# Optimization experiments

Measured on AMD Instinct MI355X. Metric: run time of the kernel, lower is better.

The kernel has to match this reference:

```python
import jax, jax.numpy as jnp
import numpy as np
from jax import lax

B, CIN, LIN = 65536, 1, 274
D, S, H, NL = 16, 18, 4, 4
DH = D // H  # 4
HID = 64
EPS = 1e-5

def layer_norm(x, g, b):
    m = jnp.mean(x, axis=-1, keepdims=True)
    v = jnp.mean(jnp.square(x - m), axis=-1, keepdims=True)
    return (x - m) * lax.rsqrt(v + EPS) * g + b

def setup_inputs() -> dict:
    key = jax.random.key(0)
    ks = jax.random.split(key, 16)
    n = lambda k, shp, s=0.05: jax.random.normal(k, shp, dtype=jnp.float32) * s
    return {
        "x": jax.random.normal(ks[0], (B, CIN, LIN), dtype=jnp.float32),
        "patch_w": n(ks[1], (D, CIN, 16), 0.2),   # Conv1d weight (O,I,K)
        "patch_b": jnp.zeros((D,), jnp.float32),
        "pos_embed": n(ks[2], (1, S, D), 0.02),
        "ln1_g": jnp.ones((NL, D), jnp.float32),
        "ln1_b": jnp.zeros((NL, D), jnp.float32),
        "qkv_w": n(ks[3], (NL, 3 * D, D), 0.2),    # in_proj_weight per layer
        "qkv_b": jnp.zeros((NL, 3 * D), jnp.float32),
        "out_w": n(ks[4], (NL, D, D), 0.2),
        "out_b": jnp.zeros((NL, D), jnp.float32),
        "ln2_g": jnp.ones((NL, D), jnp.float32),
        "ln2_b": jnp.zeros((NL, D), jnp.float32),
        "mlp_w1": n(ks[5], (NL, HID, D), 0.2),
        "mlp_b1": jnp.zeros((NL, HID), jnp.float32),
        "mlp_w2": n(ks[6], (NL, D, HID), 0.2),
        "mlp_b2": jnp.zeros((NL, D), jnp.float32),
        "lnf_g": jnp.ones((D,), jnp.float32),
        "lnf_b": jnp.zeros((D,), jnp.float32),
        "dec_w": n(ks[7], (D, CIN, 16), 0.2),      # ConvTranspose1d weight (I,O,K)
        "dec_b": jnp.zeros((CIN,), jnp.float32),
    }

def reference(x, patch_w, patch_b, pos_embed, ln1_g, ln1_b, qkv_w, qkv_b,
              out_w, out_b, ln2_g, ln2_b, mlp_w1, mlp_b1, mlp_w2, mlp_b2,
              lnf_g, lnf_b, dec_w, dec_b):
    dn = ('NCH', 'OIH', 'NCH')
    # patchify: (B,1,274) -> (B,16,18) -> (B,18,16)
    h = lax.conv_general_dilated(x, patch_w, (16,), [(7, 7)], dimension_numbers=dn)
    h = h + patch_b[None, :, None]
    h = jnp.transpose(h, (0, 2, 1)) + pos_embed
    scale = 1.0 / np.sqrt(DH)
    for i in range(NL):
        xn = layer_norm(h, ln1_g[i], ln1_b[i])
        qkv = xn @ qkv_w[i].T + qkv_b[i]                      # (B,S,3D)
        q, k, v = jnp.split(qkv, 3, axis=-1)
        q = q.reshape(B, S, H, DH)
        k = k.reshape(B, S, H, DH)
        v = v.reshape(B, S, H, DH)
        att = jnp.einsum('bqhd,bkhd->bhqk', q, k) * scale
        att = jax.nn.softmax(att, axis=-1)
        o = jnp.einsum('bhqk,bkhd->bqhd', att, v).reshape(B, S, D)
        h = h + (o @ out_w[i].T + out_b[i])
        xn2 = layer_norm(h, ln2_g[i], ln2_b[i])
        m = jax.nn.gelu(xn2 @ mlp_w1[i].T + mlp_b1[i], approximate=False)
        h = h + (m @ mlp_w2[i].T + mlp_b2[i])
    h = layer_norm(h, lnf_g, lnf_b)
    z = jnp.transpose(h, (0, 2, 1))                            # (B,16,18)
    # ConvTranspose1d(k=16, s=16, p=7): lhs_dilation=16, pad=k-1-p=8, flipped kernel
    w_t = jnp.transpose(jnp.flip(dec_w, axis=-1), (1, 0, 2))   # (O=1, I=16, 16)
    out = lax.conv_general_dilated(z, w_t, (1,), [(8, 8)], lhs_dilation=(16,),
                                   dimension_numbers=dn)
    out = out + dec_b[None, :, None]                            # (B,1,274)
    return out, z
```

## Files before the change

kernel.cpp:

```cpp
#include <hip/hip_runtime.h>
#include <math.h>
#include <stdint.h>

#define NB      65536
#define LIN     274
#define SEQ     18
#define DM      16
#define NH      4
#define HID     64
#define NLAYER  4
#define EPSF    1e-5f

#define EPB      8
#define NTHREADS 192
#define BUF_DW   3488
#define VOFF_DW  1152
#define VSTR     292
#define SMEM_DW  (2 * BUF_DW)

#define QS 0.72134752044448170f

typedef _Float16 h2    __attribute__((ext_vector_type(2)));
typedef _Float16 f16x4 __attribute__((ext_vector_type(4)));
typedef _Float16 f16x8 __attribute__((ext_vector_type(8)));
typedef float    f32x4 __attribute__((ext_vector_type(4)));
typedef __fp16   hf2_raw __attribute__((ext_vector_type(2)));

#if __has_builtin(__builtin_amdgcn_fdot2)
__device__ __forceinline__ float fdot2(h2 a, h2 b, float c) { return __builtin_amdgcn_fdot2(a, b, c, false); }
#else
__device__ __forceinline__ float fdot2(h2 a, h2 b, float c) { return c + (float)a[0] * (float)b[0] + (float)a[1] * (float)b[1]; }
#endif
#if __has_builtin(__builtin_amdgcn_cvt_pkrtz)
__device__ __forceinline__ h2 pkrtz(float a, float b) {
    hf2_raw r = __builtin_amdgcn_cvt_pkrtz(a, b);
    return __builtin_bit_cast(h2, r);
}
#else
__device__ __forceinline__ h2 pkrtz(float a, float b) { h2 r; r[0] = (_Float16)a; r[1] = (_Float16)b; return r; }
#endif

#if __has_builtin(__builtin_amdgcn_mfma_f32_16x16x16f16)
__device__ __forceinline__ f32x4 MFMA16(f16x4 a, f16x4 b, f32x4 c) {
    return __builtin_amdgcn_mfma_f32_16x16x16f16(a, b, c, 0, 0, 0);
}
#elif __has_builtin(__builtin_amdgcn_mfma_f32_16x16x16_f16)
__device__ __forceinline__ f32x4 MFMA16(f16x4 a, f16x4 b, f32x4 c) {
    return __builtin_amdgcn_mfma_f32_16x16x16_f16(a, b, c, 0, 0, 0);
}
#else
__device__ __forceinline__ f32x4 MFMA16(f16x4 a, f16x4 b, f32x4 c) {
    f32x4 d;
    asm volatile("v_mfma_f32_16x16x16_f16 %0, %1, %2, %3"
                 : "=v"(d) : "v"(a), "v"(b), "v"(c));
    return d;
}
#endif

__device__ __forceinline__ float fast_rcp(float x)  { return __builtin_amdgcn_rcpf(x); }
__device__ __forceinline__ float fast_rsq(float x)  { return __builtin_amdgcn_rsqf(x); }
__device__ __forceinline__ float fast_exp2(float x) { return __builtin_amdgcn_exp2f(x); }

__device__ __forceinline__ float bfly16_32(float x) {
#if __has_builtin(__builtin_amdgcn_permlane16_swap) && __has_builtin(__builtin_amdgcn_permlane32_swap)
    unsigned u = __builtin_bit_cast(unsigned, x);
    auto p16 = __builtin_amdgcn_permlane16_swap(u, u, false, false);
    float s = __builtin_bit_cast(float, (unsigned)p16[0]) + __builtin_bit_cast(float, (unsigned)p16[1]);
    unsigned v = __builtin_bit_cast(unsigned, s);
    auto p32 = __builtin_amdgcn_permlane32_swap(v, v, false, false);
    return __builtin_bit_cast(float, (unsigned)p32[0]) + __builtin_bit_cast(float, (unsigned)p32[1]);
#else
    x += __shfl_xor(x, 16);
    x += __shfl_xor(x, 32);
    return x;
#endif
}

__device__ __forceinline__ float gelu_tanh(float t) {
    const float A2 = 0.79788456080286536f * 2.88539008177792681f;
    const float B2 = 0.03567740814183430f * 2.88539008177792681f;
    float u  = t * fmaf(t * t, B2, A2);
    float e  = fast_exp2(u);
    float r  = fast_rcp(e + 1.0f);
    return fmaf(-t, r, t);
}

__device__ __forceinline__ f16x4 pk4(float a, float b, float c, float d) {
    h2 lo = pkrtz(a, b), hi = pkrtz(c, d);
    f16x4 r; r[0] = lo[0]; r[1] = lo[1]; r[2] = hi[0]; r[3] = hi[1];
    return r;
}
__device__ __forceinline__ f32x4 ld4(const float* p) {
    float4 t = *(const float4*)p;
    f32x4 r; r[0] = t.x; r[1] = t.y; r[2] = t.z; r[3] = t.w;
    return r;
}
__device__ __forceinline__ h2 h2at(f16x8 v, int i) {
    h2 r; r[0] = v[2 * i]; r[1] = v[2 * i + 1]; return r;
}

#define WS_H2_COUNT 6400
#define WS_BIAS_FLOATS (NLAYER * 112)
#define WS_TOTAL_BYTES (WS_H2_COUNT * 4 + WS_BIAS_FLOATS * 4)
#define PREP_ITEMS (WS_H2_COUNT + WS_BIAS_FLOATS)

__global__ __launch_bounds__(512) void prep_weights(
    const float* __restrict__ patch_w, const float* __restrict__ dec_w,
    const float* __restrict__ qkv_w, const float* __restrict__ out_w,
    const float* __restrict__ mlp_w1, const float* __restrict__ mlp_w2,
    const float* __restrict__ ln1_g, const float* __restrict__ ln1_b,
    const float* __restrict__ ln2_g, const float* __restrict__ ln2_b,
    const float* __restrict__ qkv_b, const float* __restrict__ mlp_b1,
    h2* __restrict__ ws)
{
    int i = blockIdx.x * 512 + threadIdx.x;
    if (i >= PREP_ITEMS) return;
    if (i < WS_H2_COUNT) {
        int tile = i >> 7;
        int lane = (i >> 1) & 63;
        int p    = i & 1;
        int row  = lane & 15;
        int kb   = (lane >> 4) * 4 + 2 * p;
        float a, b;
        if (tile == 0)      { a = patch_w[row * 16 + kb];  b = patch_w[row * 16 + kb + 1]; }
        else if (tile == 1) { a = dec_w[kb * 16 + row];    b = dec_w[(kb + 1) * 16 + row]; }
        else {
            int t2 = tile - 2, li = t2 / 12, j = t2 % 12;
            const float* s;
            float g0 = 1.0f, g1v = 1.0f;
            if (j < 3) {
                s = qkv_w + li * 768 + (j * 16 + row) * 16 + kb;
                g0 = ln1_g[li * 16 + kb]; g1v = ln1_g[li * 16 + kb + 1];
                if (j == 0) { g0 *= QS; g1v *= QS; }
            } else if (j == 3) {
                s = out_w + li * 256 + row * 16 + kb;
            } else if (j < 8) {
                s = mlp_w1 + li * 1024 + ((j - 4) * 16 + row) * 16 + kb;
                g0 = ln2_g[li * 16 + kb]; g1v = ln2_g[li * 16 + kb + 1];
            } else {
                s = mlp_w2 + li * 1024 + row * 64 + (j - 8) * 16 + kb;
            }
            a = s[0] * g0; b = s[1] * g1v;
        }
        ws[i] = pkrtz(a, b);
    } else {
        int t = i - WS_H2_COUNT;
        int li = t / 112, r = t % 112;
        float* wbf = (float*)(ws + WS_H2_COUNT);
        float bv;
        if (r < 48) {
            const float* Wr = qkv_w + li * 768 + r * 16;
            const float* lb = ln1_b + li * 16;
            bv = qkv_b[li * 48 + r];
            for (int d = 0; d < 16; ++d) bv = fmaf(Wr[d], lb[d], bv);
            if (r < 16) bv *= QS;
        } else {
            int j = r - 48;
            const float* Wr = mlp_w1 + li * 1024 + j * 16;
            const float* lb = ln2_b + li * 16;
            bv = mlp_b1[li * 64 + j];
            for (int d = 0; d < 16; ++d) bv = fmaf(Wr[d], lb[d], bv);
        }
        wbf[li * 112 + r] = bv;
    }
}

__global__ __launch_bounds__(NTHREADS) void ae_fwd(
    const float* __restrict__ x,
    const float* __restrict__ patch_b, const float* __restrict__ pos_embed,
    const h2*    __restrict__ wp, const float* __restrict__ wb,
    const float* __restrict__ out_b, const float* __restrict__ mlp_b2,
    const float* __restrict__ lnf_g, const float* __restrict__ lnf_b,
    const float* __restrict__ dec_b,
    float* __restrict__ out_y, float* __restrict__ out_z)
{
    __shared__ float smem[SMEM_DW];
    const int tid  = threadIdx.x;
    const int lane = tid & 63;
    const int wv   = tid >> 6;
    const int col  = lane & 15;
    const int g16  = lane >> 4;
    const int fb   = g16 * 4;

    {
        const float4* xg = (const float4*)(x + (long long)blockIdx.x * (EPB * LIN));
        float4* xs = (float4*)(smem + BUF_DW);
        for (int i = tid; i < (EPB * LIN) / 4; i += NTHREADS) xs[i] = xg[i];
    }
    __syncthreads();

    int elemL[3], sIdx[3];
    #pragma unroll
    for (int t = 0; t < 3; ++t) {
        int T = wv * 48 + t * 16 + col;
        int e = (T * 57) >> 10;
        elemL[t] = e;
        sIdx[t]  = T - 18 * e;
    }

    const f16x4* wfrag = (const f16x4*)wp;
    const f16x4 wpatch = wfrag[lane];
    const f16x4 wdec   = wfrag[64 + lane];

    float hacc[3][4];
    {
        const float4 pb = *(const float4*)(patch_b + fb);
        const float* xst = smem + BUF_DW;
        #pragma unroll
        for (int t = 0; t < 3; ++t) {
            float xv[4];
            #pragma unroll
            for (int r = 0; r < 4; ++r) {
                int loc = sIdx[t] * 16 - 7 + fb + r;
                xv[r] = (loc >= 0 && loc < LIN) ? xst[elemL[t] * LIN + loc] : 0.0f;
            }
            f16x4 xb = pk4(xv[0], xv[1], xv[2], xv[3]);
            const float4 pe = *(const float4*)(pos_embed + sIdx[t] * DM + fb);
            f32x4 c; c[0] = pb.x + pe.x; c[1] = pb.y + pe.y; c[2] = pb.z + pe.z; c[3] = pb.w + pe.w;
            c = MFMA16(wpatch, xb, c);
            #pragma unroll
            for (int r = 0; r < 4; ++r) hacc[t][r] = c[r];
        }
    }

    #pragma unroll 1
    for (int li = 0; li < NLAYER; ++li) {
        const int bufO = (li & 1) ? BUF_DW : 0;
        const f16x4* wl = wfrag + (2 + li * 12) * 64 + lane;
        const float* wbL = wb + li * 112;
        const f32x4 bq = ld4(wbL + fb);
        const f32x4 bk = ld4(wbL + 16 + fb);
        const f32x4 bvx = ld4(wbL + 32 + fb);
        f32x4 b1r[4];
        #pragma unroll
        for (int c = 0; c < 4; ++c) b1r[c] = ld4(wbL + 48 + c * 16 + fb);
        const float4 ob4 = *(const float4*)(out_b + li * DM + fb);
        const f32x4 b2r = ld4(mlp_b2 + li * DM + fb);

        h2 qp[3][2]; f16x4 kpk[3]; f32x4 vreg[3];
        #pragma unroll
        for (int t = 0; t < 3; ++t) {
            float a0 = hacc[t][0], a1 = hacc[t][1], a2 = hacc[t][2], a3 = hacc[t][3];
            float sm = bfly16_32(a0 + a1 + a2 + a3);
            float qq = bfly16_32(fmaf(a0, a0, fmaf(a1, a1, fmaf(a2, a2, a3 * a3))));
            float mean = sm * (1.0f / 16.0f);
            float var  = fmaxf(fmaf(mean, -mean, qq * (1.0f / 16.0f)), 0.0f);
            float inv  = fast_rsq(var + EPSF);
            float mi   = mean * inv;
            f16x4 xb = pk4(fmaf(a0, inv, -mi), fmaf(a1, inv, -mi),
                           fmaf(a2, inv, -mi), fmaf(a3, inv, -mi));
            f32x4 aq = MFMA16(wl[0],   xb, bq);
            f32x4 ak = MFMA16(wl[64],  xb, bk);
            f32x4 av = MFMA16(wl[128], xb, bvx);
            qp[t][0] = pkrtz(aq[0], aq[1]);
            qp[t][1] = pkrtz(aq[2], aq[3]);
            kpk[t] = pk4(ak[0], ak[1], ak[2], ak[3]);
            vreg[t] = av;
        }
        #pragma unroll
        for (int t = 0; t < 3; ++t) {
            ((f16x4*)(smem + bufO))[(elemL[t] * 4 + g16) * 18 + sIdx[t]] = kpk[t];
            float4 vv; vv.x = vreg[t][0]; vv.y = vreg[t][1]; vv.z = vreg[t][2]; vv.w = vreg[t][3];
            *(float4*)(smem + bufO + VOFF_DW + elemL[t] * VSTR + sIdx[t] * 16 + g16 * 4) = vv;
        }
        __syncthreads();

        #pragma unroll
        for (int t = 0; t < 3; ++t) {
            const int e = elemL[t];
            const f16x4* Kb = (const f16x4*)(smem + bufO) + (e * 4 + g16) * 18;
            float sc[SEQ]; float ssum = 0.0f;
            #pragma unroll
            for (int jp = 0; jp < 9; ++jp) {
                f16x8 k2 = *(const f16x8*)(Kb + 2 * jp);
                float s0 = fdot2(qp[t][1], h2at(k2, 1), fdot2(qp[t][0], h2at(k2, 0), 0.0f));
                float s1 = fdot2(qp[t][1], h2at(k2, 3), fdot2(qp[t][0], h2at(k2, 2), 0.0f));
                float w0 = fast_exp2(s0), w1 = fast_exp2(s1);
                sc[2 * jp] = w0; sc[2 * jp + 1] = w1;
                ssum += w0 + w1;
            }
            float inv = fast_rcp(ssum);
            const float* vb = smem + bufO + VOFF_DW + e * VSTR + g16 * 4;
            float o0 = 0.f, o1 = 0.f, o2 = 0.f, o3 = 0.f;
            #pragma unroll
            for (int j = 0; j < SEQ; ++j) {
                float4 vj = *(const float4*)(vb + j * 16);
                float w = sc[j];
                o0 = fmaf(w, vj.x, o0); o1 = fmaf(w, vj.y, o1);
                o2 = fmaf(w, vj.z, o2); o3 = fmaf(w, vj.w, o3);
            }
            f16x4 obf = pk4(o0 * inv, o1 * inv, o2 * inv, o3 * inv);
            f32x4 oa; oa[0] = ob4.x; oa[1] = ob4.y; oa[2] = ob4.z; oa[3] = ob4.w;
            oa = MFMA16(wl[192], obf, oa);
            #pragma unroll
            for (int r = 0; r < 4; ++r) hacc[t][r] += oa[r];
        }

        #pragma unroll
        for (int t = 0; t < 3; ++t) {
            float a0 = hacc[t][0], a1 = hacc[t][1], a2 = hacc[t][2], a3 = hacc[t][3];
            float sm = bfly16_32(a0 + a1 + a2 + a3);
            float qq = bfly16_32(fmaf(a0, a0, fmaf(a1, a1, fmaf(a2, a2, a3 * a3))));
            float mean = sm * (1.0f / 16.0f);
            float var  = fmaxf(fmaf(mean, -mean, qq * (1.0f / 16.0f)), 0.0f);
            float inv  = fast_rsq(var + EPSF);
            float mi   = mean * inv;
            f16x4 xb2 = pk4(fmaf(a0, inv, -mi), fmaf(a1, inv, -mi),
                            fmaf(a2, inv, -mi), fmaf(a3, inv, -mi));
            f32x4 acc2 = b2r;
            #pragma unroll
            for (int c = 0; c < 4; ++c) {
                f32x4 m1 = MFMA16(wl[(4 + c) * 64], xb2, b1r[c]);
                f16x4 gb = pk4(gelu_tanh(m1[0]), gelu_tanh(m1[1]),
                               gelu_tanh(m1[2]), gelu_tanh(m1[3]));
                acc2 = MFMA16(wl[(8 + c) * 64], gb, acc2);
            }
            #pragma unroll
            for (int r = 0; r < 4; ++r) hacc[t][r] += acc2[r];
        }
    }

    const float4 gf = *(const float4*)(lnf_g + fb);
    const float4 bf = *(const float4*)(lnf_b + fb);
    const float db0 = dec_b[0];
    #pragma unroll
    for (int t = 0; t < 3; ++t) {
        float a0 = hacc[t][0], a1 = hacc[t][1], a2 = hacc[t][2], a3 = hacc[t][3];
        float sm = bfly16_32(a0 + a1 + a2 + a3);
        float qq = bfly16_32(fmaf(a0, a0, fmaf(a1, a1, fmaf(a2, a2, a3 * a3))));
        float mean = sm * (1.0f / 16.0f);
        float var  = fmaxf(fmaf(mean, -mean, qq * (1.0f / 16.0f)), 0.0f);
        float inv  = fast_rsq(var + EPSF);
        float mi   = mean * inv;
        float f0 = fmaf(fmaf(a0, inv, -mi), gf.x, bf.x);
        float f1 = fmaf(fmaf(a1, inv, -mi), gf.y, bf.y);
        float f2 = fmaf(fmaf(a2, inv, -mi), gf.z, bf.z);
        float f3 = fmaf(fmaf(a3, inv, -mi), gf.w, bf.w);

        long long eg = (long long)blockIdx.x * EPB + elemL[t];
        float* zb = out_z + eg * (DM * SEQ) + sIdx[t];
        zb[(fb + 0) * SEQ] = f0; zb[(fb + 1) * SEQ] = f1;
        zb[(fb + 2) * SEQ] = f2; zb[(fb + 3) * SEQ] = f3;

        f16x4 hb = pk4(f0, f1, f2, f3);
        f32x4 y4; y4[0] = db0; y4[1] = db0; y4[2] = db0; y4[3] = db0;
        y4 = MFMA16(wdec, hb, y4);
        float* yb = out_y + eg * LIN;
        int p0 = sIdx[t] * 16 + fb - 7;
        #pragma unroll
        for (int r = 0; r < 4; ++r) {
            int p = p0 + r;
            if (p >= 0 && p < LIN) yb[p] = y4[r];
        }
    }
}

#define EPB_F 14
#define NT_F  252
__global__ __launch_bounds__(NT_F) void ae_fwd_f32(
    const float* __restrict__ x,
    const float* __restrict__ patch_w, const float* __restrict__ patch_b,
    const float* __restrict__ pos_embed,
    const float* __restrict__ ln1_g, const float* __restrict__ ln1_b,
    const float* __restrict__ qkv_w, const float* __restrict__ qkv_b,
    const float* __restrict__ out_w, const float* __restrict__ out_b,
    const float* __restrict__ ln2_g, const float* __restrict__ ln2_b,
    const float* __restrict__ mlp_w1, const float* __restrict__ mlp_b1,
    const float* __restrict__ mlp_w2, const float* __restrict__ mlp_b2,
    const float* __restrict__ lnf_g, const float* __restrict__ lnf_b,
    const float* __restrict__ dec_w, const float* __restrict__ dec_b,
    float* __restrict__ out_y, float* __restrict__ out_z)
{
    __shared__ float s_kv[EPB_F * 580];
    const int tid = threadIdx.x;
    const int e   = tid / SEQ;
    const int s   = tid - e * SEQ;
    const long long b = (long long)blockIdx.x * EPB_F + e;
    const bool valid = (b < NB);
    {
        const long long base = (long long)blockIdx.x * (EPB_F * LIN);
        const long long lim  = (long long)NB * LIN - 1;
        for (int i = tid; i < EPB_F * LIN; i += NT_F) {
            long long gi = base + i;
            if (gi > lim) gi = lim;
            s_kv[i] = x[gi];
        }
    }
    __syncthreads();
    float xv[16];
    {
        const float* xe = &s_kv[e * LIN];
        #pragma unroll
        for (int k = 0; k < 16; ++k) {
            int idx = s * 16 - 7 + k;
            xv[k] = (idx >= 0 && idx < LIN) ? xe[idx] : 0.0f;
        }
    }
    float h[DM];
    #pragma unroll
    for (int d = 0; d < DM; ++d) {
        float acc = patch_b[d] + pos_embed[s * DM + d];
        #pragma unroll
        for (int k = 0; k < 16; ++k) acc = fmaf(xv[k], patch_w[d * 16 + k], acc);
        h[d] = acc;
    }
    #pragma unroll 1
    for (int li = 0; li < NLAYER; ++li) {
        float xn[DM];
        {
            float m = 0.f;
            #pragma unroll
            for (int d = 0; d < DM; ++d) m += h[d];
            m *= (1.0f / DM);
            float v = 0.f;
            #pragma unroll
            for (int d = 0; d < DM; ++d) { float t = h[d] - m; v = fmaf(t, t, v); }
            v *= (1.0f / DM);
            float inv = fast_rsq(v + EPSF);
            #pragma unroll
            for (int d = 0; d < DM; ++d) xn[d] = (h[d] - m) * inv * ln1_g[li * DM + d] + ln1_b[li * DM + d];
        }
        float q[DM], kk[DM], vv[DM];
        {
            const float* W  = qkv_w + li * 48 * DM;
            const float* Wb = qkv_b + li * 48;
            #pragma unroll
            for (int j = 0; j < DM; ++j) {
                float aq = Wb[j], ak = Wb[DM + j], av = Wb[2 * DM + j];
                #pragma unroll
                for (int d = 0; d < DM; ++d) {
                    float xd = xn[d];
                    aq = fmaf(xd, W[j * DM + d], aq);
                    ak = fmaf(xd, W[(DM + j) * DM + d], ak);
                    av = fmaf(xd, W[(2 * DM + j) * DM + d], av);
                }
                q[j] = aq; kk[j] = ak; vv[j] = av;
            }
        }
        __syncthreads();
        {
            float* kb = &s_kv[e * 580];
            float* vb = kb + SEQ * DM;
            #pragma unroll
            for (int j = 0; j < DM; ++j) kb[s * DM + j] = kk[j];
            #pragma unroll
            for (int j = 0; j < DM; ++j) vb[s * DM + j] = vv[j];
        }
        __syncthreads();
        float o[DM];
        {
            const float* kb = &s_kv[e * 580];
            const float* vb = kb + SEQ * DM;
            #pragma unroll
            for (int hh = 0; hh < NH; ++hh) {
                const float qscale = 0.5f * 1.44269504088896341f;
                const float q0 = q[hh * 4] * qscale, q1 = q[hh * 4 + 1] * qscale;
                const float q2 = q[hh * 4 + 2] * qscale, q3 = q[hh * 4 + 3] * qscale;
                float sc[SEQ];
                float ssum = 0.f;
                #pragma unroll
                for (int j = 0; j < SEQ; ++j) {
                    const float4 kj = *(const float4*)(kb + j * DM + hh * 4);
                    float t = fmaf(q0, kj.x, fmaf(q1, kj.y, fmaf(q2, kj.z, q3 * kj.w)));
                    float w = fast_exp2(t);
                    sc[j] = w; ssum += w;
                }
                const float inv = fast_rcp(ssum);
                float a0 = 0.f, a1 = 0.f, a2 = 0.f, a3 = 0.f;
                #pragma unroll
                for (int j = 0; j < SEQ; ++j) {
                    const float4 vj = *(const float4*)(vb + j * DM + hh * 4);
                    const float w = sc[j] * inv;
                    a0 = fmaf(w, vj.x, a0); a1 = fmaf(w, vj.y, a1);
                    a2 = fmaf(w, vj.z, a2); a3 = fmaf(w, vj.w, a3);
                }
                o[hh * 4] = a0; o[hh * 4 + 1] = a1; o[hh * 4 + 2] = a2; o[hh * 4 + 3] = a3;
            }
        }
        {
            const float* W  = out_w + li * DM * DM;
            #pragma unroll
            for (int d = 0; d < DM; ++d) {
                float acc = out_b[li * DM + d];
                #pragma unroll
                for (int d2 = 0; d2 < DM; ++d2) acc = fmaf(o[d2], W[d * DM + d2], acc);
                h[d] += acc;
            }
        }
        float xn2[DM];
        {
            float m = 0.f;
            #pragma unroll
            for (int d = 0; d < DM; ++d) m += h[d];
            m *= (1.0f / DM);
            float v = 0.f;
            #pragma unroll
            for (int d = 0; d < DM; ++d) { float t = h[d] - m; v = fmaf(t, t, v); }
            v *= (1.0f / DM);
            float inv = fast_rsq(v + EPSF);
            #pragma unroll
            for (int d = 0; d < DM; ++d) xn2[d] = (h[d] - m) * inv * ln2_g[li * DM + d] + ln2_b[li * DM + d];
        }
        {
            const float* W1 = mlp_w1 + li * HID * DM;
            const float* W2 = mlp_w2 + li * DM * HID;
            float acc2[DM];
            #pragma unroll
            for (int d = 0; d < DM; ++d) acc2[d] = mlp_b2[li * DM + d];
            #pragma unroll 2
            for (int j = 0; j < HID; ++j) {
                float t = mlp_b1[li * HID + j];
                #pragma unroll
                for (int d = 0; d < DM; ++d) t = fmaf(xn2[d], W1[j * DM + d], t);
                float g = gelu_tanh(t);
                #pragma unroll
                for (int d = 0; d < DM; ++d) acc2[d] = fmaf(g, W2[d * HID + j], acc2[d]);
            }
            #pragma unroll
            for (int d = 0; d < DM; ++d) h[d] += acc2[d];
        }
    }
    {
        float m = 0.f;
        #pragma unroll
        for (int d = 0; d < DM; ++d) m += h[d];
        m *= (1.0f / DM);
        float v = 0.f;
        #pragma unroll
        for (int d = 0; d < DM; ++d) { float t = h[d] - m; v = fmaf(t, t, v); }
        v *= (1.0f / DM);
        float inv = fast_rsq(v + EPSF);
        #pragma unroll
        for (int d = 0; d < DM; ++d) h[d] = (h[d] - m) * inv * lnf_g[d] + lnf_b[d];
    }
    if (valid) {
        float* zb = out_z + b * (DM * SEQ);
        #pragma unroll
        for (int d = 0; d < DM; ++d) zb[d * SEQ + s] = h[d];
        float* yb = out_y + b * LIN;
        const float db0 = dec_b[0];
        #pragma unroll
        for (int k = 0; k < 16; ++k) {
            int t = s * 16 + k - 7;
            if (t >= 0 && t < LIN) {
                float acc = db0;
                #pragma unroll
                for (int d = 0; d < DM; ++d) acc = fmaf(h[d], dec_w[d * 16 + k], acc);
                yb[t] = acc;
            }
        }
    }
}

extern "C" void kernel_launch(void* const* d_in, const int* in_sizes, int n_in,
                              void* d_out, int out_size, void* d_ws, size_t ws_size,
                              hipStream_t stream) {
    const float* x        = (const float*)d_in[0];
    const float* patch_w  = (const float*)d_in[1];
    const float* patch_b  = (const float*)d_in[2];
    const float* pos_e    = (const float*)d_in[3];
    const float* ln1_g    = (const float*)d_in[4];
    const float* ln1_b    = (const float*)d_in[5];
    const float* qkv_w    = (const float*)d_in[6];
    const float* qkv_b    = (const float*)d_in[7];
    const float* out_w    = (const float*)d_in[8];
    const float* out_b    = (const float*)d_in[9];
    const float* ln2_g    = (const float*)d_in[10];
    const float* ln2_b    = (const float*)d_in[11];
    const float* mlp_w1   = (const float*)d_in[12];
    const float* mlp_b1   = (const float*)d_in[13];
    const float* mlp_w2   = (const float*)d_in[14];
    const float* mlp_b2   = (const float*)d_in[15];
    const float* lnf_g    = (const float*)d_in[16];
    const float* lnf_b    = (const float*)d_in[17];
    const float* dec_w    = (const float*)d_in[18];
    const float* dec_b    = (const float*)d_in[19];

    float* out_y = (float*)d_out;
    float* out_z = out_y + (long long)NB * LIN;

    if (ws_size >= WS_TOTAL_BYTES) {
        h2* wsp = (h2*)d_ws;
        const float* wbp = (const float*)(wsp + WS_H2_COUNT);
        prep_weights<<<(PREP_ITEMS + 511) / 512, 512, 0, stream>>>(
            patch_w, dec_w, qkv_w, out_w, mlp_w1, mlp_w2,
            ln1_g, ln1_b, ln2_g, ln2_b, qkv_b, mlp_b1, wsp);
        ae_fwd<<<NB / EPB, NTHREADS, 0, stream>>>(
            x, patch_b, pos_e, wsp, wbp,
            out_b, mlp_b2, lnf_g, lnf_b, dec_b, out_y, out_z);
    } else {
        const int grid = (NB + EPB_F - 1) / EPB_F;
        ae_fwd_f32<<<grid, NT_F, 0, stream>>>(
            x, patch_w, patch_b, pos_e, ln1_g, ln1_b, qkv_w, qkv_b,
            out_w, out_b, ln2_g, ln2_b, mlp_w1, mlp_b1, mlp_w2, mlp_b2,
            lnf_g, lnf_b, dec_w, dec_b, out_y, out_z);
    }
}
```

Baseline: 492.7 us.

## Run each block as a single wavefront and drop all block barriers

Each block becomes one 64-lane wavefront that handles all 144 tokens of its 8 elements, so each lane carries nine token tiles instead of three. Because K and V are produced and consumed by the same wave, the __syncthreads barriers and the double-buffered shared memory go away. V is now stored as fp16 with a padded layout, which shrinks LDS to 2592 dwords and allows more blocks per CU, and weight fragments are hoisted out of the per-token loops. In exchange, register pressure rises sharply with hacc[9][4] and qp[9][2], and the launch bound requests 3 waves per EU, which risks spills.

```diff
diff --git a/kernel.cpp b/kernel.cpp
--- a/kernel.cpp
+++ b/kernel.cpp
@@ -12,11 +12,9 @@
 #define EPSF    1e-5f
 
 #define EPB      8
-#define NTHREADS 192
-#define BUF_DW   3488
+#define NTHREADS 64
 #define VOFF_DW  1152
-#define VSTR     292
-#define SMEM_DW  (2 * BUF_DW)
+#define SMEM_DW  2592
 
 #define QS 0.72134752044448170f
 
@@ -165,7 +163,7 @@
     }
 }
 
-__global__ __launch_bounds__(NTHREADS) void ae_fwd(
+__global__ __launch_bounds__(NTHREADS, 3) void ae_fwd(
     const float* __restrict__ x,
     const float* __restrict__ patch_b, const float* __restrict__ pos_embed,
     const h2*    __restrict__ wp, const float* __restrict__ wb,
@@ -175,24 +173,25 @@
     float* __restrict__ out_y, float* __restrict__ out_z)
 {
     __shared__ float smem[SMEM_DW];
-    const int tid  = threadIdx.x;
-    const int lane = tid & 63;
-    const int wv   = tid >> 6;
+    const int lane = threadIdx.x;
     const int col  = lane & 15;
     const int g16  = lane >> 4;
     const int fb   = g16 * 4;
 
     {
         const float4* xg = (const float4*)(x + (long long)blockIdx.x * (EPB * LIN));
-        float4* xs = (float4*)(smem + BUF_DW);
-        for (int i = tid; i < (EPB * LIN) / 4; i += NTHREADS) xs[i] = xg[i];
-    }
-    __syncthreads();
-
-    int elemL[3], sIdx[3];
+        float4* xs = (float4*)smem;
+        #pragma unroll
+        for (int i = 0; i < 9; ++i) {
+            int idx = lane + i * 64;
+            if (idx < (EPB * LIN) / 4) xs[idx] = xg[idx];
+        }
+    }
+
+    int elemL[9], sIdx[9];
     #pragma unroll
-    for (int t = 0; t < 3; ++t) {
-        int T = wv * 48 + t * 16 + col;
+    for (int t = 0; t < 9; ++t) {
+        int T = t * 16 + col;
         int e = (T * 57) >> 10;
         elemL[t] = e;
         sIdx[t]  = T - 18 * e;
@@ -200,19 +199,17 @@
 
     const f16x4* wfrag = (const f16x4*)wp;
     const f16x4 wpatch = wfrag[lane];
-    const f16x4 wdec   = wfrag[64 + lane];
-
-    float hacc[3][4];
+
+    float hacc[9][4];
     {
         const float4 pb = *(const float4*)(patch_b + fb);
-        const float* xst = smem + BUF_DW;
-        #pragma unroll
-        for (int t = 0; t < 3; ++t) {
+        #pragma unroll
+        for (int t = 0; t < 9; ++t) {
             float xv[4];
             #pragma unroll
             for (int r = 0; r < 4; ++r) {
                 int loc = sIdx[t] * 16 - 7 + fb + r;
-                xv[r] = (loc >= 0 && loc < LIN) ? xst[elemL[t] * LIN + loc] : 0.0f;
+                xv[r] = (loc >= 0 && loc < LIN) ? smem[elemL[t] * LIN + loc] : 0.0f;
             }
             f16x4 xb = pk4(xv[0], xv[1], xv[2], xv[3]);
             const float4 pe = *(const float4*)(pos_embed + sIdx[t] * DM + fb);
@@ -225,106 +222,114 @@
 
     #pragma unroll 1
     for (int li = 0; li < NLAYER; ++li) {
-        const int bufO = (li & 1) ? BUF_DW : 0;
         const f16x4* wl = wfrag + (2 + li * 12) * 64 + lane;
         const float* wbL = wb + li * 112;
-        const f32x4 bq = ld4(wbL + fb);
-        const f32x4 bk = ld4(wbL + 16 + fb);
-        const f32x4 bvx = ld4(wbL + 32 + fb);
-        f32x4 b1r[4];
-        #pragma unroll
-        for (int c = 0; c < 4; ++c) b1r[c] = ld4(wbL + 48 + c * 16 + fb);
-        const float4 ob4 = *(const float4*)(out_b + li * DM + fb);
-        const f32x4 b2r = ld4(mlp_b2 + li * DM + fb);
-
-        h2 qp[3][2]; f16x4 kpk[3]; f32x4 vreg[3];
-        #pragma unroll
-        for (int t = 0; t < 3; ++t) {
-            float a0 = hacc[t][0], a1 = hacc[t][1], a2 = hacc[t][2], a3 = hacc[t][3];
-            float sm = bfly16_32(a0 + a1 + a2 + a3);
-            float qq = bfly16_32(fmaf(a0, a0, fmaf(a1, a1, fmaf(a2, a2, a3 * a3))));
-            float mean = sm * (1.0f / 16.0f);
-            float var  = fmaxf(fmaf(mean, -mean, qq * (1.0f / 16.0f)), 0.0f);
-            float inv  = fast_rsq(var + EPSF);
-            float mi   = mean * inv;
-            f16x4 xb = pk4(fmaf(a0, inv, -mi), fmaf(a1, inv, -mi),
-                           fmaf(a2, inv, -mi), fmaf(a3, inv, -mi));
-            f32x4 aq = MFMA16(wl[0],   xb, bq);
-            f32x4 ak = MFMA16(wl[64],  xb, bk);
-            f32x4 av = MFMA16(wl[128], xb, bvx);
-            qp[t][0] = pkrtz(aq[0], aq[1]);
-            qp[t][1] = pkrtz(aq[2], aq[3]);
-            kpk[t] = pk4(ak[0], ak[1], ak[2], ak[3]);
-            vreg[t] = av;
-        }
-        #pragma unroll
-        for (int t = 0; t < 3; ++t) {
-            ((f16x4*)(smem + bufO))[(elemL[t] * 4 + g16) * 18 + sIdx[t]] = kpk[t];
-            float4 vv; vv.x = vreg[t][0]; vv.y = vreg[t][1]; vv.z = vreg[t][2]; vv.w = vreg[t][3];
-            *(float4*)(smem + bufO + VOFF_DW + elemL[t] * VSTR + sIdx[t] * 16 + g16 * 4) = vv;
-        }
-        __syncthreads();
-
-        #pragma unroll
-        for (int t = 0; t < 3; ++t) {
-            const int e = elemL[t];
-            const f16x4* Kb = (const f16x4*)(smem + bufO) + (e * 4 + g16) * 18;
-            float sc[SEQ]; float ssum = 0.0f;
-            #pragma unroll
-            for (int jp = 0; jp < 9; ++jp) {
-                f16x8 k2 = *(const f16x8*)(Kb + 2 * jp);
-                float s0 = fdot2(qp[t][1], h2at(k2, 1), fdot2(qp[t][0], h2at(k2, 0), 0.0f));
-                float s1 = fdot2(qp[t][1], h2at(k2, 3), fdot2(qp[t][0], h2at(k2, 2), 0.0f));
-                float w0 = fast_exp2(s0), w1 = fast_exp2(s1);
-                sc[2 * jp] = w0; sc[2 * jp + 1] = w1;
-                ssum += w0 + w1;
-            }
-            float inv = fast_rcp(ssum);
-            const float* vb = smem + bufO + VOFF_DW + e * VSTR + g16 * 4;
-            float o0 = 0.f, o1 = 0.f, o2 = 0.f, o3 = 0.f;
-            #pragma unroll
-            for (int j = 0; j < SEQ; ++j) {
-                float4 vj = *(const float4*)(vb + j * 16);
-                float w = sc[j];
-                o0 = fmaf(w, vj.x, o0); o1 = fmaf(w, vj.y, o1);
-                o2 = fmaf(w, vj.z, o2); o3 = fmaf(w, vj.w, o3);
-            }
-            f16x4 obf = pk4(o0 * inv, o1 * inv, o2 * inv, o3 * inv);
-            f32x4 oa; oa[0] = ob4.x; oa[1] = ob4.y; oa[2] = ob4.z; oa[3] = ob4.w;
-            oa = MFMA16(wl[192], obf, oa);
-            #pragma unroll
-            for (int r = 0; r < 4; ++r) hacc[t][r] += oa[r];
-        }
-
-        #pragma unroll
-        for (int t = 0; t < 3; ++t) {
-            float a0 = hacc[t][0], a1 = hacc[t][1], a2 = hacc[t][2], a3 = hacc[t][3];
-            float sm = bfly16_32(a0 + a1 + a2 + a3);
-            float qq = bfly16_32(fmaf(a0, a0, fmaf(a1, a1, fmaf(a2, a2, a3 * a3))));
-            float mean = sm * (1.0f / 16.0f);
-            float var  = fmaxf(fmaf(mean, -mean, qq * (1.0f / 16.0f)), 0.0f);
-            float inv  = fast_rsq(var + EPSF);
-            float mi   = mean * inv;
-            f16x4 xb2 = pk4(fmaf(a0, inv, -mi), fmaf(a1, inv, -mi),
-                            fmaf(a2, inv, -mi), fmaf(a3, inv, -mi));
-            f32x4 acc2 = b2r;
+
+        h2 qp[9][2];
+        {
+            const f32x4 bq  = ld4(wbL + fb);
+            const f32x4 bk  = ld4(wbL + 16 + fb);
+            const f32x4 bvx = ld4(wbL + 32 + fb);
+            const f16x4 wq = wl[0], wk = wl[64], wvw = wl[128];
+            #pragma unroll
+            for (int t = 0; t < 9; ++t) {
+                float a0 = hacc[t][0], a1 = hacc[t][1], a2 = hacc[t][2], a3 = hacc[t][3];
+                float sm = bfly16_32(a0 + a1 + a2 + a3);
+                float qq = bfly16_32(fmaf(a0, a0, fmaf(a1, a1, fmaf(a2, a2, a3 * a3))));
+                float mean = sm * (1.0f / 16.0f);
+                float var  = fmaxf(fmaf(mean, -mean, qq * (1.0f / 16.0f)), 0.0f);
+                float inv  = fast_rsq(var + EPSF);
+                float mi   = mean * inv;
+                f16x4 xb = pk4(fmaf(a0, inv, -mi), fmaf(a1, inv, -mi),
+                               fmaf(a2, inv, -mi), fmaf(a3, inv, -mi));
+                f32x4 aq = MFMA16(wq,  xb, bq);
+                f32x4 ak = MFMA16(wk,  xb, bk);
+                f32x4 av = MFMA16(wvw, xb, bvx);
+                qp[t][0] = pkrtz(aq[0], aq[1]);
+                qp[t][1] = pkrtz(aq[2], aq[3]);
+                *(f16x4*)(smem + (elemL[t] * 4 + g16) * 36 + sIdx[t] * 2) =
+                    pk4(ak[0], ak[1], ak[2], ak[3]);
+                *(f16x4*)(smem + VOFF_DW + (elemL[t] * 18 + sIdx[t]) * 10 + g16 * 2) =
+                    pk4(av[0], av[1], av[2], av[3]);
+            }
+        }
+
+        {
+            const float4 ob4 = *(const float4*)(out_b + li * DM + fb);
+            const f16x4 wo = wl[192];
+            #pragma unroll
+            for (int t = 0; t < 9; ++t) {
+                const float* Kb = smem + (elemL[t] * 4 + g16) * 36;
+                float sc[SEQ]; float ssum = 0.0f;
+                #pragma unroll
+                for (int jp = 0; jp < 9; ++jp) {
+                    f16x8 k2 = *(const f16x8*)(Kb + jp * 4);
+                    float s0 = fdot2(qp[t][1], h2at(k2, 1), fdot2(qp[t][0], h2at(k2, 0), 0.0f));
+                    float s1 = fdot2(qp[t][1], h2at(k2, 3), fdot2(qp[t][0], h2at(k2, 2), 0.0f));
+                    float w0 = fast_exp2(s0), w1 = fast_exp2(s1);
+                    sc[2 * jp] = w0; sc[2 * jp + 1] = w1;
+                    ssum += w0 + w1;
+                }
+                float inv = fast_rcp(ssum);
+                const float* vbase = smem + VOFF_DW + elemL[t] * 180 + g16 * 2;
+                float o0 = 0.f, o1 = 0.f, o2 = 0.f, o3 = 0.f;
+                #pragma unroll
+                for (int j = 0; j < SEQ; ++j) {
+                    f16x4 vj = *(const f16x4*)(vbase + j * 10);
+                    float w = sc[j];
+                    o0 = fmaf(w, (float)vj[0], o0);
+                    o1 = fmaf(w, (float)vj[1], o1);
+                    o2 = fmaf(w, (float)vj[2], o2);
+                    o3 = fmaf(w, (float)vj[3], o3);
+                }
+                f16x4 obf = pk4(o0 * inv, o1 * inv, o2 * inv, o3 * inv);
+                f32x4 oa; oa[0] = ob4.x; oa[1] = ob4.y; oa[2] = ob4.z; oa[3] = ob4.w;
+                oa = MFMA16(wo, obf, oa);
+                #pragma unroll
+                for (int r = 0; r < 4; ++r) hacc[t][r] += oa[r];
+            }
+        }
+
+        {
+            f32x4 b1r[4]; f16x4 w1c[4], w2c[4];
             #pragma unroll
             for (int c = 0; c < 4; ++c) {
-                f32x4 m1 = MFMA16(wl[(4 + c) * 64], xb2, b1r[c]);
-                f16x4 gb = pk4(gelu_tanh(m1[0]), gelu_tanh(m1[1]),
-                               gelu_tanh(m1[2]), gelu_tanh(m1[3]));
-                acc2 = MFMA16(wl[(8 + c) * 64], gb, acc2);
-            }
-            #pragma unroll
-            for (int r = 0; r < 4; ++r) hacc[t][r] += acc2[r];
-        }
-    }
-
+                b1r[c] = ld4(wbL + 48 + c * 16 + fb);
+                w1c[c] = wl[(4 + c) * 64];
+                w2c[c] = wl[(8 + c) * 64];
+            }
+            const f32x4 b2r = ld4(mlp_b2 + li * DM + fb);
+            #pragma unroll
+            for (int t = 0; t < 9; ++t) {
+                float a0 = hacc[t][0], a1 = hacc[t][1], a2 = hacc[t][2], a3 = hacc[t][3];
+                float sm = bfly16_32(a0 + a1 + a2 + a3);
+                float qq = bfly16_32(fmaf(a0, a0, fmaf(a1, a1, fmaf(a2, a2, a3 * a3))));
+                float mean = sm * (1.0f / 16.0f);
+                float var  = fmaxf(fmaf(mean, -mean, qq * (1.0f / 16.0f)), 0.0f);
+                float inv  = fast_rsq(var + EPSF);
+                float mi   = mean * inv;
+                f16x4 xb2 = pk4(fmaf(a0, inv, -mi), fmaf(a1, inv, -mi),
+                                fmaf(a2, inv, -mi), fmaf(a3, inv, -mi));
+                f32x4 acc2 = b2r;
+                #pragma unroll
+                for (int c = 0; c < 4; ++c) {
+                    f32x4 m1 = MFMA16(w1c[c], xb2, b1r[c]);
+                    f16x4 gb = pk4(gelu_tanh(m1[0]), gelu_tanh(m1[1]),
+                                   gelu_tanh(m1[2]), gelu_tanh(m1[3]));
+                    acc2 = MFMA16(w2c[c], gb, acc2);
+                }
+                #pragma unroll
+                for (int r = 0; r < 4; ++r) hacc[t][r] += acc2[r];
+            }
+        }
+    }
+
+    const f16x4 wdec = wfrag[64 + lane];
     const float4 gf = *(const float4*)(lnf_g + fb);
     const float4 bf = *(const float4*)(lnf_b + fb);
     const float db0 = dec_b[0];
     #pragma unroll
-    for (int t = 0; t < 3; ++t) {
+    for (int t = 0; t < 9; ++t) {
         float a0 = hacc[t][0], a1 = hacc[t][1], a2 = hacc[t][2], a3 = hacc[t][3];
         float sm = bfly16_32(a0 + a1 + a2 + a3);
         float qq = bfly16_32(fmaf(a0, a0, fmaf(a1, a1, fmaf(a2, a2, a3 * a3))));
```

Measured after the change: 460.3 us. 1.07x faster.
